# Kernel tuning notes

Hardware: AMD Instinct MI355X
Metric: run time of the kernel (lower is better)

## Reference

```python
import jax, jax.numpy as jnp
from jax import lax
import numpy as np

BS = 16      # gather block size (with halo)
ST = 14      # block stride == output block size (16 - 3 + 1)
TOL = 0.5


def setup_inputs() -> dict:
    key = jax.random.key(0)
    k1, k2, k3 = jax.random.split(key, 3)
    N, H, W, Cin, Cout = 8, 506, 506, 32, 32
    x = jax.random.normal(k1, (N, H, W, Cin), dtype=jnp.float32)
    mask = jax.random.uniform(k2, (N, H, W, 1), dtype=jnp.float32)
    kernel = jax.random.normal(k3, (3, 3, Cin, Cout), dtype=jnp.float32) * 0.05
    bias = jnp.zeros((Cout,), dtype=jnp.float32)
    return {"x": x, "mask": mask, "kernel": kernel, "bias": bias}


def _gather_blocks(t, ridx, cidx):
    # t: [N,H,W,C] -> [N, nbh, BS, nbw, BS, C]
    return t[:, ridx][:, :, :, cidx]


def reference(x, mask, kernel, bias):
    N, H, W, Cin = x.shape
    Cout = kernel.shape[-1]
    nbh = (H - BS) // ST + 1
    nbw = (W - BS) // ST + 1
    ridx = jnp.arange(nbh)[:, None] * ST + jnp.arange(BS)[None, :]  # [nbh,BS]
    cidx = jnp.arange(nbw)[:, None] * ST + jnp.arange(BS)[None, :]  # [nbw,BS]

    # reduce_mask: per-block max pool (avgpool=False), active iff > tol
    mblk = _gather_blocks(mask, ridx, cidx)            # [N,nbh,BS,nbw,BS,1]
    active = jnp.max(mblk, axis=(2, 4))[..., 0] > TOL  # [N,nbh,nbw] bool

    # sparse_gather: extract overlapping 16x16 blocks (stride 14, 1px halo)
    blk = _gather_blocks(x, ridx, cidx)                # [N,nbh,BS,nbw,BS,Cin]
    blk = blk.transpose(0, 1, 3, 2, 4, 5).reshape(N * nbh * nbw, BS, BS, Cin)

    # dense conv on blocks ('same' padding, as in the original Conv2D layer)
    y = lax.conv_general_dilated(
        blk, kernel, window_strides=(1, 1), padding="SAME",
        dimension_numbers=("NHWC", "HWIO", "NHWC")) + bias

    # interior 14x14 (halo makes it equal to dense valid conv there)
    y = y[:, 1:1 + ST, 1:1 + ST, :]                    # [NB,14,14,Cout]

    # sparse_scatter into a zeros tensor: inactive blocks stay zero
    y = y.reshape(N, nbh, nbw, ST, ST, Cout)
    y = y * active[..., None, None, None].astype(y.dtype)
    out = y.transpose(0, 1, 3, 2, 4, 5).reshape(N, nbh * ST, nbw * ST, Cout)
    return out  # [N, H-2, W-2, Cout]
```

## Files before the change

### kernel.cpp

```cpp
#include <hip/hip_runtime.h>


#define BS   16
#define ST   14
#define NBH  36
#define NBW  36
#define NN   8
#define HH   506
#define WW   506
#define CIN  32
#define COUT 32
#define OH   504
#define OW   504

#define XS_CI_STRIDE 260

__global__ __launch_bounds__(448) void sparse_conv_kernel(
    const float* __restrict__ x, const float* __restrict__ mask,
    const float* __restrict__ kern, const float* __restrict__ bias,
    float* __restrict__ out)
{
    __shared__ float xs[CIN * XS_CI_STRIDE];
    __shared__ float sred[8];
    __shared__ float sflag;

    const int bw = blockIdx.x, bh = blockIdx.y, n = blockIdx.z;
    const int t  = threadIdx.x;
    const int r0 = bh * ST, c0 = bw * ST;

    float m = 0.0f;
    if (t < 256) {
        const int i = t >> 4, j = t & 15;
        m = mask[(size_t)(n * HH + r0 + i) * WW + (c0 + j)];
    }
    #pragma unroll
    for (int off = 32; off > 0; off >>= 1)
        m = fmaxf(m, __shfl_down(m, off, 64));
    if ((t & 63) == 0) sred[t >> 6] = m;
    __syncthreads();
    if (t == 0) {
        const float mm = fmaxf(fmaxf(sred[0], sred[1]), fmaxf(sred[2], sred[3]));
        sflag = (mm > 0.5f) ? 1.0f : 0.0f;
    }

    for (int q = t; q < 2048; q += 448) {
        const int r = q >> 7;
        const int o = q & 127;
        const int c = o >> 3;
        const int ci4 = o & 7;
        const float4 v = *(const float4*)(
            x + ((size_t)(n * HH + r0 + r) * WW + (c0 + c)) * CIN + ci4 * 4);
        float* p = &xs[(ci4 * 4) * XS_CI_STRIDE + r * 16 + c];
        p[0]                = v.x;
        p[XS_CI_STRIDE]     = v.y;
        p[2 * XS_CI_STRIDE] = v.z;
        p[3 * XS_CI_STRIDE] = v.w;
    }
    __syncthreads();

    const float flag = sflag;
    const int co = t & 31;
    const int g  = t >> 5;

    float acc[14];
    #pragma unroll
    for (int i = 0; i < 14; ++i) acc[i] = 0.0f;

    for (int dr = 0; dr < 3; ++dr) {
        const int r = g + dr;
        for (int ci = 0; ci < 32; ++ci) {
            const float4* xr4 = (const float4*)&xs[ci * XS_CI_STRIDE + r * 16];
            const float4 v0 = xr4[0], v1 = xr4[1], v2 = xr4[2], v3 = xr4[3];
            float xv[16];
            xv[0]=v0.x; xv[1]=v0.y; xv[2]=v0.z; xv[3]=v0.w;
            xv[4]=v1.x; xv[5]=v1.y; xv[6]=v1.z; xv[7]=v1.w;
            xv[8]=v2.x; xv[9]=v2.y; xv[10]=v2.z; xv[11]=v2.w;
            xv[12]=v3.x; xv[13]=v3.y; xv[14]=v3.z; xv[15]=v3.w;
            #pragma unroll
            for (int dc = 0; dc < 3; ++dc) {
                const float k = kern[((dr * 3 + dc) * 32 + ci) * 32 + co];
                #pragma unroll
                for (int oj = 0; oj < 14; ++oj)
                    acc[oj] = fmaf(xv[oj + dc], k, acc[oj]);
            }
        }
    }

    const float bv = bias[co];
    const size_t obase = ((size_t)(n * OH + r0 + g) * OW + c0) * COUT + co;
    #pragma unroll
    for (int oj = 0; oj < 14; ++oj)
        out[obase + (size_t)oj * COUT] = (acc[oj] + bv) * flag;
}

extern "C" void kernel_launch(void* const* d_in, const int* in_sizes, int n_in,
                              void* d_out, int out_size, void* d_ws, size_t ws_size,
                              hipStream_t stream) {
    const float* x    = (const float*)d_in[0];
    const float* mask = (const float*)d_in[1];
    const float* kern = (const float*)d_in[2];
    const float* bias = (const float*)d_in[3];
    float* out        = (float*)d_out;

    dim3 grid(NBW, NBH, NN);
    sparse_conv_kernel<<<grid, 448, 0, stream>>>(x, mask, kern, bias, out);
}
```

Before: 885.3 us.

## Split mask reduction into separate kernel and retile conv as dense 16x16 pixel tiles

Moves the per-block mask max into its own small kernel that writes flags to workspace. The convolution becomes a dense 16x16 output tile per workgroup with an 18x18 halo, channel-last in shared memory. Each thread computes all 32 output channels for one pixel, reads weights uniformly from global memory, and issues float4 stores. This aims to improve weight reuse and store coalescing and to drop redundant halo loads. The costs are an extra launch, 32 accumulators per thread, and weight loads streamed through the scalar/cache path.

```diff
diff --git a/kernel.cpp b/kernel.cpp
--- a/kernel.cpp
+++ b/kernel.cpp
@@ -1,38 +1,24 @@
 #include <hip/hip_runtime.h>
 
 
-#define BS   16
-#define ST   14
-#define NBH  36
-#define NBW  36
-#define NN   8
-#define HH   506
-#define WW   506
-#define CIN  32
-#define COUT 32
-#define OH   504
-#define OW   504
+#define NN    8
+#define HH    506
+#define WW    506
+#define CIN   32
+#define COUT  32
+#define OH    504
+#define OW    504
+#define NBH   36
+#define NBW   36
 
-#define XS_CI_STRIDE 260
-
-__global__ __launch_bounds__(448) void sparse_conv_kernel(
-    const float* __restrict__ x, const float* __restrict__ mask,
-    const float* __restrict__ kern, const float* __restrict__ bias,
-    float* __restrict__ out)
+__global__ __launch_bounds__(256) void mask_flags_kernel(
+    const float* __restrict__ mask, float* __restrict__ flags)
 {
-    __shared__ float xs[CIN * XS_CI_STRIDE];
-    __shared__ float sred[8];
-    __shared__ float sflag;
-
+    __shared__ float sred[4];
     const int bw = blockIdx.x, bh = blockIdx.y, n = blockIdx.z;
-    const int t  = threadIdx.x;
-    const int r0 = bh * ST, c0 = bw * ST;
-
-    float m = 0.0f;
-    if (t < 256) {
-        const int i = t >> 4, j = t & 15;
-        m = mask[(size_t)(n * HH + r0 + i) * WW + (c0 + j)];
-    }
+    const int t = threadIdx.x;
+    const int i = t >> 4, j = t & 15;
+    float m = mask[(size_t)(n * HH + bh * 14 + i) * WW + (bw * 14 + j)];
     #pragma unroll
     for (int off = 32; off > 0; off >>= 1)
         m = fmaxf(m, __shfl_down(m, off, 64));
@@ -40,57 +26,80 @@
     __syncthreads();
     if (t == 0) {
         const float mm = fmaxf(fmaxf(sred[0], sred[1]), fmaxf(sred[2], sred[3]));
-        sflag = (mm > 0.5f) ? 1.0f : 0.0f;
+        flags[(n * NBH + bh) * NBW + bw] = (mm > 0.5f) ? 1.0f : 0.0f;
     }
+}
 
-    for (int q = t; q < 2048; q += 448) {
-        const int r = q >> 7;
-        const int o = q & 127;
-        const int c = o >> 3;
-        const int ci4 = o & 7;
+#define TO 16
+#define TI 18
+#define PS 36
+
+__global__ __launch_bounds__(256) void conv16_kernel(
+    const float* __restrict__ x, const float* __restrict__ kern,
+    const float* __restrict__ bias, const float* __restrict__ flags,
+    float* __restrict__ out)
+{
+    __shared__ float xs[TI * TI * PS];
+
+    const int bx = blockIdx.x, by = blockIdx.y, n = blockIdx.z;
+    const int R0 = by * TO, C0 = bx * TO;
+    const int t = threadIdx.x;
+
+    for (int q = t; q < TI * TI * 8; q += 256) {
+        const int row = q / (TI * 8);
+        const int rem = q - row * (TI * 8);
+        const int c = rem >> 3, g = rem & 7;
+        const int gr = min(R0 + row, HH - 1);
+        const int gc = min(C0 + c, WW - 1);
         const float4 v = *(const float4*)(
-            x + ((size_t)(n * HH + r0 + r) * WW + (c0 + c)) * CIN + ci4 * 4);
-        float* p = &xs[(ci4 * 4) * XS_CI_STRIDE + r * 16 + c];
-        p[0]                = v.x;
-        p[XS_CI_STRIDE]     = v.y;
-        p[2 * XS_CI_STRIDE] = v.z;
-        p[3 * XS_CI_STRIDE] = v.w;
+            x + ((size_t)(n * HH + gr) * WW + gc) * CIN + g * 4);
+        *(float4*)&xs[(row * TI + c) * PS + g * 4] = v;
     }
     __syncthreads();
 
-    const float flag = sflag;
-    const int co = t & 31;
-    const int g  = t >> 5;
+    const int i = t >> 4, j = t & 15;
 
-    float acc[14];
+    float acc[COUT];
     #pragma unroll
-    for (int i = 0; i < 14; ++i) acc[i] = 0.0f;
+    for (int co = 0; co < COUT; ++co) acc[co] = 0.0f;
 
+    #pragma unroll 1
     for (int dr = 0; dr < 3; ++dr) {
-        const int r = g + dr;
-        for (int ci = 0; ci < 32; ++ci) {
-            const float4* xr4 = (const float4*)&xs[ci * XS_CI_STRIDE + r * 16];
-            const float4 v0 = xr4[0], v1 = xr4[1], v2 = xr4[2], v3 = xr4[3];
-            float xv[16];
-            xv[0]=v0.x; xv[1]=v0.y; xv[2]=v0.z; xv[3]=v0.w;
-            xv[4]=v1.x; xv[5]=v1.y; xv[6]=v1.z; xv[7]=v1.w;
-            xv[8]=v2.x; xv[9]=v2.y; xv[10]=v2.z; xv[11]=v2.w;
-            xv[12]=v3.x; xv[13]=v3.y; xv[14]=v3.z; xv[15]=v3.w;
+        #pragma unroll 1
+        for (int dc = 0; dc < 3; ++dc) {
+            const float4* xp = (const float4*)&xs[((i + dr) * TI + (j + dc)) * PS];
+            float xv[CIN];
             #pragma unroll
-            for (int dc = 0; dc < 3; ++dc) {
-                const float k = kern[((dr * 3 + dc) * 32 + ci) * 32 + co];
+            for (int g = 0; g < 8; ++g) {
+                const float4 v = xp[g];
+                xv[g * 4 + 0] = v.x; xv[g * 4 + 1] = v.y;
+                xv[g * 4 + 2] = v.z; xv[g * 4 + 3] = v.w;
+            }
+            const float* kp = kern + (dr * 3 + dc) * (CIN * COUT);
+            #pragma unroll
+            for (int ci = 0; ci < CIN; ++ci) {
+                const float xc = xv[ci];
                 #pragma unroll
-                for (int oj = 0; oj < 14; ++oj)
-                    acc[oj] = fmaf(xv[oj + dc], k, acc[oj]);
+                for (int co = 0; co < COUT; ++co)
+                    acc[co] = fmaf(xc, kp[ci * COUT + co], acc[co]);
             }
         }
     }
 
-    const float bv = bias[co];
-    const size_t obase = ((size_t)(n * OH + r0 + g) * OW + c0) * COUT + co;
-    #pragma unroll
-    for (int oj = 0; oj < 14; ++oj)
-        out[obase + (size_t)oj * COUT] = (acc[oj] + bv) * flag;
+    const int r = R0 + i, c = C0 + j;
+    if (r < OH && c < OW) {
+        const float flag = flags[((size_t)n * NBH + r / 14) * NBW + c / 14];
+        float* op = out + ((size_t)(n * OH + r) * OW + c) * COUT;
+        #pragma unroll
+        for (int g = 0; g < 8; ++g) {
+            float4 v;
+            v.x = (acc[g * 4 + 0] + bias[g * 4 + 0]) * flag;
+            v.y = (acc[g * 4 + 1] + bias[g * 4 + 1]) * flag;
+            v.z = (acc[g * 4 + 2] + bias[g * 4 + 2]) * flag;
+            v.w = (acc[g * 4 + 3] + bias[g * 4 + 3]) * flag;
+            *(float4*)(op + g * 4) = v;
+        }
+    }
 }
 
 extern "C" void kernel_launch(void* const* d_in, const int* in_sizes, int n_in,
@@ -101,7 +110,11 @@
     const float* kern = (const float*)d_in[2];
     const float* bias = (const float*)d_in[3];
     float* out        = (float*)d_out;
+    float* flags      = (float*)d_ws;
 
-    dim3 grid(NBW, NBH, NN);
-    sparse_conv_kernel<<<grid, 448, 0, stream>>>(x, mask, kern, bias, out);
+    dim3 gridA(NBW, NBH, NN);
+    mask_flags_kernel<<<gridA, 256, 0, stream>>>(mask, flags);
+
+    dim3 gridB((OW + TO - 1) / TO, (OH + TO - 1) / TO, NN);
+    conv16_kernel<<<gridB, 256, 0, stream>>>(x, kern, bias, flags, out);
 }
```

Result: slower. 1.014 ms (+14.6%).
